# Kernel tuning notes

Hardware: AMD Instinct MI355X
Metric: run time of the kernel (lower is better)

Reference implementation:

```python
import jax, jax.numpy as jnp
import numpy as np

B, T, C, H, N = 4, 4096, 2048, 32, 64
DMIX, DDEC = 32, 64
N_LAYER, LAYER_ID = 24, 12
GN_EPS = 1e-5 * 8.0 ** 2  # eps = 1e-5 * head_size_divisor**2


def setup_inputs() -> dict:
    key = jax.random.key(0)
    ks = jax.random.split(key, 24)
    r01 = LAYER_ID / (N_LAYER - 1)
    r1a0 = 1.0 - LAYER_ID / N_LAYER
    ddd = (np.arange(C, dtype=np.float32) / C).reshape(1, 1, C)
    maa = lambda p: jnp.asarray(1.0 - ddd ** p, dtype=jnp.float32)
    # decay speed schedule (canonical RWKV6, over channel dim)
    n = np.arange(C, dtype=np.float32)
    decay = (-6.0 + 5.0 * (n / (C - 1)) ** (0.7 + 1.3 * r01)).reshape(1, 1, C)
    # time_faaaa zigzag schedule
    m = np.arange(C, dtype=np.float32)
    zig = ((m + 1) % 3 - 1) * 0.1
    faaaa = (r01 * (1 - m / (C - 1)) + zig).reshape(H, N)
    s = 1.0 / np.sqrt(C)
    return {
        "x": jax.random.normal(ks[0], (B, T, C), jnp.float32),
        "shift_state": jax.random.normal(ks[1], (B, C), jnp.float32),
        "wkv_state": jnp.zeros((B, H, N, N), jnp.float32),
        "time_maa_x": maa(r1a0),
        "time_maa_w": maa(r1a0),
        "time_maa_k": maa(r1a0),
        "time_maa_v": jnp.asarray(1.0 - (ddd ** r1a0 + 0.3 * r01), jnp.float32),
        "time_maa_r": maa(0.5 * r1a0),
        "time_maa_g": maa(0.5 * r1a0),
        "time_maa_w1": jax.random.normal(ks[2], (C, 5 * DMIX), jnp.float32) * 0.01,
        "time_maa_w2": jax.random.uniform(ks[3], (5, DMIX, C), jnp.float32, -0.01, 0.01),
        "time_decay": jnp.asarray(decay, jnp.float32),
        "time_decay_w1": jax.random.normal(ks[4], (C, DDEC), jnp.float32) * 0.01,
        "time_decay_w2": jax.random.uniform(ks[5], (DDEC, C), jnp.float32, -0.01, 0.01),
        "time_faaaa": jnp.asarray(faaaa, jnp.float32),
        "Wr": jax.random.normal(ks[6], (C, C), jnp.float32) * s,
        "Wk": jax.random.normal(ks[7], (C, C), jnp.float32) * s,
        "Wv": jax.random.normal(ks[8], (C, C), jnp.float32) * s,
        "Wg": jax.random.normal(ks[9], (C, C), jnp.float32) * s,
        "Wo": jax.random.normal(ks[10], (C, C), jnp.float32) * s,
        "gn_weight": jnp.ones((C,), jnp.float32),
        "gn_bias": jnp.zeros((C,), jnp.float32),
    }


def reference(x, shift_state, wkv_state, time_maa_x, time_maa_w, time_maa_k,
              time_maa_v, time_maa_r, time_maa_g, time_maa_w1, time_maa_w2,
              time_decay, time_decay_w1, time_decay_w2, time_faaaa,
              Wr, Wk, Wv, Wg, Wo, gn_weight, gn_bias):
    b, t, c = x.shape
    # token shift: previous token (seeded by shift_state) minus current
    xx = jnp.concatenate([shift_state[:, None, :], x[:, :-1]], axis=1) - x
    lx = x[:, -1]
    # LoRA token-shift mixing
    xxx = x + xx * time_maa_x
    t5 = jnp.tanh(xxx @ time_maa_w1).reshape(b, t, 5, DMIX)
    mixes = jnp.einsum('btfd,fdc->fbtc', t5, time_maa_w2)
    mw, mk, mv, mr, mg = mixes
    xw = x + xx * (time_maa_w + mw)
    xk = x + xx * (time_maa_k + mk)
    xv = x + xx * (time_maa_v + mv)
    xr = x + xx * (time_maa_r + mr)
    xg = x + xx * (time_maa_g + mg)
    r = xr @ Wr
    k = xk @ Wk
    v = xv @ Wv
    g = jax.nn.silu(xg @ Wg)
    # data-dependent decay via LoRA; wkv6 uses log-decay -exp(w)
    w = time_decay + jnp.tanh(xw @ time_decay_w1) @ time_decay_w2
    glog = -jnp.exp(w)  # [b,t,c]
    to_heads = lambda z: z.reshape(b, t, H, N).transpose(1, 0, 2, 3)  # [t,b,h,n]
    rh, kh, vh, gh = to_heads(r), to_heads(k), to_heads(v), to_heads(glog)
    u = time_faaaa  # [H,N]

    def step(S, inp):
        r_t, k_t, v_t, g_t = inp  # each [b,h,n]
        kv = jnp.einsum('bhk,bhv->bhkv', k_t, v_t)
        o_t = jnp.einsum('bhk,bhkv->bhv', r_t, S + u[None, :, :, None] * kv)
        S = jnp.exp(g_t)[..., None] * S + kv
        return S, o_t

    state, o = jax.lax.scan(step, wkv_state, (rh, kh, vh, gh))
    o = o.transpose(1, 0, 2, 3).reshape(b, t, c)  # [b,t,c]
    # GroupNorm with H groups over channel dim
    og = o.reshape(b, t, H, N)
    mu = og.mean(-1, keepdims=True)
    var = og.var(-1, keepdims=True)
    on = (og - mu) * jax.lax.rsqrt(var + GN_EPS)
    on = on * gn_weight.reshape(H, N) + gn_bias.reshape(H, N)
    out = (on.reshape(b, t, c) * g) @ Wo
    return out, lx, state
```

## Files before the change

kernel.cpp:

```cpp
#include <hip/hip_runtime.h>
#include <hip/hip_bf16.h>
#include <stdint.h>

#define DEV __device__ __forceinline__

typedef __bf16 bf16x8 __attribute__((ext_vector_type(8)));
typedef float f32x4 __attribute__((ext_vector_type(4)));
typedef unsigned short u16x8 __attribute__((ext_vector_type(8)));

constexpr int kB = 4, kT = 4096, kC = 2048, kH = 32, kN = 64;
constexpr int kM = kB * kT;
constexpr int SEGN = 8, TSEG = kT / SEGN, CHN = TSEG / 64;

DEV float bfu2f(unsigned short u) {
  union { uint32_t i; float f; } x; x.i = ((uint32_t)u) << 16; return x.f;
}
DEV unsigned short f2bfu(float f) {
  union { float f; uint32_t i; } x; x.f = f;
  uint32_t r = x.i + 0x7FFFu + ((x.i >> 16) & 1u);
  return (unsigned short)(r >> 16);
}

DEV void gld16(const void* g, void* l) {
  __builtin_amdgcn_global_load_lds(
      (const __attribute__((address_space(1))) void*)g,
      (__attribute__((address_space(3))) void*)l, 16, 0, 0);
}

DEV int swzb(int row, int byteoff) { return (row << 7) + (byteoff ^ ((row & 7) << 4)); }

__global__ __launch_bounds__(256) void trans_bf16(
    const float* __restrict__ in, unsigned short* __restrict__ out, int R, int Cn) {
  __shared__ __attribute__((aligned(16))) unsigned short tile[64][65];
  const int t = threadIdx.x;
  const int r0 = blockIdx.y * 64, c0 = blockIdx.x * 64;
  const int lr = t >> 6, lc = t & 63;
#pragma unroll
  for (int i = 0; i < 16; i++) {
    int rr = lr + i * 4;
    int gr = r0 + rr, gc = c0 + lc;
    if (gr < R && gc < Cn) tile[rr][lc] = f2bfu(in[(size_t)gr * Cn + gc]);
  }
  __syncthreads();
#pragma unroll
  for (int i = 0; i < 16; i++) {
    int cc = lr + i * 4;
    int gc = c0 + cc, gr = r0 + lc;
    if (gc < Cn && gr < R) out[(size_t)gc * R + gr] = tile[lc][cc];
  }
}

__global__ __launch_bounds__(256) void prep_x2(
    const float* __restrict__ x, const float* __restrict__ shift,
    const float* __restrict__ maax,
    unsigned short* __restrict__ xxx, float* __restrict__ lx) {
  size_t i4 = ((size_t)blockIdx.x * 256 + threadIdx.x) * 4;
  int c = (int)(i4 & (kC - 1));
  size_t bt = i4 >> 11;
  int tt = (int)(bt & (kT - 1));
  int b = (int)(bt >> 12);
  float4 xv = *(const float4*)(x + i4);
  float4 pv = (tt == 0) ? *(const float4*)(shift + (size_t)b * kC + c)
                        : *(const float4*)(x + i4 - kC);
  float4 mx = *(const float4*)(maax + c);
  ushort4 o4;
  o4.x = f2bfu(xv.x + (pv.x - xv.x) * mx.x);
  o4.y = f2bfu(xv.y + (pv.y - xv.y) * mx.y);
  o4.z = f2bfu(xv.z + (pv.z - xv.z) * mx.z);
  o4.w = f2bfu(xv.w + (pv.w - xv.w) * mx.w);
  *(ushort4*)(xxx + i4) = o4;
  if (tt == kT - 1) *(float4*)(lx + (size_t)b * kC + c) = xv;
}

enum { E_F32 = 0, E_BF16 = 1, E_TANH = 2, E_SILU = 3, E_DECAY = 4 };

template <int BM, int BN, int EPI>
__global__ __launch_bounds__(256) void gemm_k(
    const unsigned short* __restrict__ A, const unsigned short* __restrict__ Bt,
    void* __restrict__ Cout, const float* __restrict__ aux, int M, int N, int K) {
  constexpr int WGM = (BM == 128 && BN == 128) ? 2 : (BM == 64 ? 2 : 4);
  constexpr int WGN = 4 / WGM;
  constexpr int WM = BM / WGM, WN = BN / WGN;
  constexpr int WR = WM / 16, WC = WN / 16;
  __shared__ __attribute__((aligned(16))) unsigned short As[BM * 32];
  __shared__ __attribute__((aligned(16))) unsigned short Bs[BN * 32];
  const int t = threadIdx.x, wid = t >> 6, l = t & 63;
  const int m0 = blockIdx.x * BM, n0 = blockIdx.y * BN;
  const int wm0 = (wid / WGN) * WM, wn0 = (wid % WGN) * WN;
  f32x4 acc[WR][WC];
#pragma unroll
  for (int i = 0; i < WR; i++)
#pragma unroll
    for (int j = 0; j < WC; j++) acc[i][j] = f32x4{0.f, 0.f, 0.f, 0.f};

  const int rowS = t >> 2, cbS = (t & 3) * 16;
  const char* Ab = (const char*)A;
  const char* Bb = (const char*)Bt;
  const int aoff = (wm0 + (l & 15)) * 32 + (l >> 4) * 8;
  const int boff = (wn0 + (l & 15)) * 32 + (l >> 4) * 8;

  for (int kt = 0; kt < K; kt += 32) {
#pragma unroll
    for (int ia = 0; ia < BM / 64; ia++)
      gld16(Ab + ((size_t)(m0 + ia * 64 + rowS) * K + kt) * 2 + cbS,
            (char*)As + ia * 4096 + wid * 1024);
    if constexpr (BN >= 64) {
#pragma unroll
      for (int ib = 0; ib < BN / 64; ib++)
        gld16(Bb + ((size_t)(n0 + ib * 64 + rowS) * K + kt) * 2 + cbS,
              (char*)Bs + ib * 4096 + wid * 1024);
    } else {
      if (t < BN * 4)
        gld16(Bb + ((size_t)(n0 + rowS) * K + kt) * 2 + cbS,
              (char*)Bs + wid * 1024);
    }
    __syncthreads();
    bf16x8 af[WR], bfv[WC];
#pragma unroll
    for (int mi = 0; mi < WR; mi++) af[mi] = *(const bf16x8*)(&As[aoff + mi * 512]);
#pragma unroll
    for (int ni = 0; ni < WC; ni++) bfv[ni] = *(const bf16x8*)(&Bs[boff + ni * 512]);
#pragma unroll
    for (int mi = 0; mi < WR; mi++)
#pragma unroll
      for (int ni = 0; ni < WC; ni++)
        acc[mi][ni] = __builtin_amdgcn_mfma_f32_16x16x32_bf16(af[mi], bfv[ni], acc[mi][ni], 0, 0, 0);
    __syncthreads();
  }

#pragma unroll
  for (int mi = 0; mi < WR; mi++) {
#pragma unroll
    for (int ni = 0; ni < WC; ni++) {
      int row = m0 + wm0 + mi * 16 + (l >> 4) * 4;
      int col = n0 + wn0 + ni * 16 + (l & 15);
#pragma unroll
      for (int j = 0; j < 4; j++) {
        float v = acc[mi][ni][j];
        size_t idx = (size_t)(row + j) * N + col;
        if constexpr (EPI == E_F32) ((float*)Cout)[idx] = v;
        else if constexpr (EPI == E_BF16) ((unsigned short*)Cout)[idx] = f2bfu(v);
        else if constexpr (EPI == E_TANH) ((unsigned short*)Cout)[idx] = f2bfu(tanhf(v));
        else if constexpr (EPI == E_SILU) ((unsigned short*)Cout)[idx] = f2bfu(v / (1.f + expf(-v)));
        else if constexpr (EPI == E_DECAY) {
          float w = v + aux[col];
          ((float*)Cout)[idx] = expf(-expf(w));
        }
      }
    }
  }
}

DEV void stage256(const unsigned short* A, const unsigned short* Bt,
                  char* lds, int aoff, int boff, int m0, int n0, int K, int kt,
                  int tid, int wid) {
#pragma unroll
  for (int i = 0; i < 4; i++) {
    int row = i * 64 + (tid >> 3);
    int cb = ((tid & 7) * 16) ^ ((row & 7) << 4);
    gld16((const char*)A + ((size_t)(m0 + row) * K + kt) * 2 + cb,
          lds + aoff + i * 8192 + wid * 1024);
    gld16((const char*)Bt + ((size_t)(n0 + row) * K + kt) * 2 + cb,
          lds + boff + i * 8192 + wid * 1024);
  }
}

template <int EPI>
__global__ __launch_bounds__(512, 2) void gemm256_k(
    const unsigned short* __restrict__ A, const unsigned short* __restrict__ Bt,
    void* __restrict__ Cout, int M, int N, int K) {
  extern __shared__ __attribute__((aligned(16))) char lds[];
  const int tid = threadIdx.x, wid = tid >> 6, l = tid & 63;

  const int nwg = gridDim.x, cpx = nwg >> 3;
  int swz = (blockIdx.x & 7) * cpx + (blockIdx.x >> 3);
  const int mtiles = M >> 8;
  const int m0 = (swz % mtiles) * 256, n0 = (swz / mtiles) * 256;

  const int wm = (wid >> 2) * 128, wn = (wid & 3) * 64;
  f32x4 acc[8][4];
#pragma unroll
  for (int i = 0; i < 8; i++)
#pragma unroll
    for (int j = 0; j < 4; j++) acc[i][j] = f32x4{0.f, 0.f, 0.f, 0.f};

  const int KT = K >> 6;
  stage256(A, Bt, lds, 0, 65536, m0, n0, K, 0, tid, wid);
  __syncthreads();
  int cur = 0;

  for (int t = 0; t < KT; ++t) {
    if (t + 1 < KT)
      stage256(A, Bt, lds, (cur ^ 1) * 32768, 65536 + (cur ^ 1) * 32768,
               m0, n0, K, (t + 1) * 64, tid, wid);
    const char* Ab = lds + cur * 32768;
    const char* Bb = lds + 65536 + cur * 32768;
    __builtin_amdgcn_s_setprio(1);
#pragma unroll
    for (int ks = 0; ks < 2; ks++) {
      bf16x8 a[8];
#pragma unroll
      for (int mi = 0; mi < 8; mi++)
        a[mi] = *(const bf16x8*)(Ab + swzb(wm + mi * 16 + (l & 15), ks * 64 + (l >> 4) * 16));
#pragma unroll
      for (int ni = 0; ni < 4; ni++) {
        bf16x8 b = *(const bf16x8*)(Bb + swzb(wn + ni * 16 + (l & 15), ks * 64 + (l >> 4) * 16));
#pragma unroll
        for (int mi = 0; mi < 8; mi++)
          acc[mi][ni] = __builtin_amdgcn_mfma_f32_16x16x32_bf16(a[mi], b, acc[mi][ni], 0, 0, 0);
      }
    }
    __builtin_amdgcn_s_setprio(0);
    __syncthreads();
    cur ^= 1;
  }

#pragma unroll
  for (int mi = 0; mi < 8; mi++)
#pragma unroll
    for (int ni = 0; ni < 4; ni++) {
      int row = m0 + wm + mi * 16 + (l >> 4) * 4;
      int col = n0 + wn + ni * 16 + (l & 15);
#pragma unroll
      for (int j = 0; j < 4; j++) {
        float v = acc[mi][ni][j];
        size_t idx = (size_t)(row + j) * N + col;
        if constexpr (EPI == E_F32) ((float*)Cout)[idx] = v;
        else if constexpr (EPI == E_BF16) ((unsigned short*)Cout)[idx] = f2bfu(v);
        else if constexpr (EPI == E_SILU) ((unsigned short*)Cout)[idx] = f2bfu(v / (1.f + expf(-v)));
      }
    }
}

__global__ __launch_bounds__(256) void mixf_k(
    const unsigned short* __restrict__ t5, const unsigned short* __restrict__ w2t,
    const float* __restrict__ x, const float* __restrict__ shift,
    const float* __restrict__ maa, unsigned short* __restrict__ xout, int f) {
  __shared__ __attribute__((aligned(16))) unsigned short As[64 * 32];
  __shared__ __attribute__((aligned(16))) unsigned short Bs[64 * 32];
  const int t = threadIdx.x, wid = t >> 6, l = t & 63;
  const int m0 = blockIdx.x * 64, n0 = blockIdx.y * 64;
  const int wm0 = (wid >> 1) * 32, wn0 = (wid & 1) * 32;
  const int rowS = t >> 2, cbS = (t & 3) * 16;
  const int aoff = (wm0 + (l & 15)) * 32 + (l >> 4) * 8;
  const int boff = (wn0 + (l & 15)) * 32 + (l >> 4) * 8;

  gld16((const char*)t5 + ((size_t)(m0 + rowS) * 160 + f * 32) * 2 + cbS, (char*)As + wid * 1024);
  gld16((const char*)w2t + ((size_t)(n0 + rowS) * 160 + f * 32) * 2 + cbS, (char*)Bs + wid * 1024);
  __syncthreads();
  bf16x8 a0 = *(const bf16x8*)(&As[aoff]), a1 = *(const bf16x8*)(&As[aoff + 512]);
  bf16x8 b0 = *(const bf16x8*)(&Bs[boff]), b1 = *(const bf16x8*)(&Bs[boff + 512]);
  f32x4 acc[2][2];
  acc[0][0] = f32x4{0.f, 0.f, 0.f, 0.f}; acc[0][1] = f32x4{0.f, 0.f, 0.f, 0.f};
  acc[1][0] = f32x4{0.f, 0.f, 0.f, 0.f}; acc[1][1] = f32x4{0.f, 0.f, 0.f, 0.f};
  acc[0][0] = __builtin_amdgcn_mfma_f32_16x16x32_bf16(a0, b0, acc[0][0], 0, 0, 0);
  acc[0][1] = __builtin_amdgcn_mfma_f32_16x16x32_bf16(a0, b1, acc[0][1], 0, 0, 0);
  acc[1][0] = __builtin_amdgcn_mfma_f32_16x16x32_bf16(a1, b0, acc[1][0], 0, 0, 0);
  acc[1][1] = __builtin_amdgcn_mfma_f32_16x16x32_bf16(a1, b1, acc[1][1], 0, 0, 0);

#pragma unroll
  for (int mi = 0; mi < 2; mi++)
#pragma unroll
    for (int ni = 0; ni < 2; ni++) {
      int row = m0 + wm0 + mi * 16 + (l >> 4) * 4;
      int col = n0 + wn0 + ni * 16 + (l & 15);
      float mv = maa[col];
#pragma unroll
      for (int j = 0; j < 4; j++) {
        int rrow = row + j;
        int tt = rrow & (kT - 1);
        size_t idx = (size_t)rrow * kC + col;
        float xv = x[idx];
        float pv = (tt == 0) ? shift[(size_t)(rrow >> 12) * kC + col] : x[idx - kC];
        xout[idx] = f2bfu(xv + (pv - xv) * (mv + acc[mi][ni][j]));
      }
    }
}

__global__ __launch_bounds__(256) void wkv_local_k(
    const unsigned short* __restrict__ kb, const unsigned short* __restrict__ vb,
    const float* __restrict__ ed, float* __restrict__ Lbuf, float* __restrict__ Dseg) {
  const int bid = blockIdx.x;
  const int bh = bid >> 3, seg = bid & 7;
  const int h = bh & 31, b = bh >> 5;
  const int tid = threadIdx.x, w = tid >> 6, l = tid & 63;
  __shared__ __attribute__((aligned(16))) unsigned short KQks[4096];
  __shared__ __attribute__((aligned(16))) unsigned short Vt[4096];
  __shared__ __attribute__((aligned(16))) float Sf[64][68];
  __shared__ float segp[4][64];
  __shared__ float DLs[64];

  const int fr = l & 15, fq = l >> 4;
#pragma unroll
  for (int ni = 0; ni < 4; ni++)
#pragma unroll
    for (int j = 0; j < 4; j++) Sf[w * 16 + fq * 4 + j][ni * 16 + fr] = 0.f;

  float dtot = 1.f;
  float kv[16], dv[16], vv[16];
  {
    size_t g = ((size_t)b * kT + seg * TSEG + w * 16) * kC + h * 64 + l;
#pragma unroll
    for (int i = 0; i < 16; i++) {
      kv[i] = bfu2f(kb[g]); vv[i] = bfu2f(vb[g]); dv[i] = ed[g];
      g += kC;
    }
  }

  for (int ch = 0; ch < CHN; ++ch) {
    float p = 1.f;
#pragma unroll
    for (int i = 0; i < 16; i++) p *= dv[i];
    segp[w][l] = p;
    __syncthreads();
    float pre = 1.f;
    if (w > 0) pre *= segp[0][l];
    if (w > 1) pre *= segp[1][l];
    if (w > 2) pre *= segp[2][l];
    if (w == 3) DLs[l] = pre * p;

    unsigned short kqrow[16], vtrow[16];
    float run = pre;
#pragma unroll
    for (int i = 0; i < 16; i++) {
      run *= dv[i];
      kqrow[i] = f2bfu(kv[i] / run);
      vtrow[i] = f2bfu(vv[i]);
    }
    {
      u16x8 q0, q1, v0, v1;
#pragma unroll
      for (int j = 0; j < 8; j++) { q0[j] = kqrow[j]; q1[j] = kqrow[j + 8]; v0[j] = vtrow[j]; v1[j] = vtrow[j + 8]; }
      *(u16x8*)((char*)KQks + swzb(l, w * 32)) = q0;
      *(u16x8*)((char*)KQks + swzb(l, w * 32 + 16)) = q1;
      *(u16x8*)((char*)Vt + swzb(l, w * 32)) = v0;
      *(u16x8*)((char*)Vt + swzb(l, w * 32 + 16)) = v1;
    }
    if (ch < CHN - 1) {
      size_t g = ((size_t)b * kT + seg * TSEG + (ch + 1) * 64 + w * 16) * kC + h * 64 + l;
#pragma unroll
      for (int i = 0; i < 16; i++) {
        kv[i] = bfu2f(kb[g]); vv[i] = bfu2f(vb[g]); dv[i] = ed[g];
        g += kC;
      }
    }
    __syncthreads();

    bf16x8 kA0 = *(const bf16x8*)((const char*)KQks + swzb(w * 16 + fr, fq * 16));
    bf16x8 kA1 = *(const bf16x8*)((const char*)KQks + swzb(w * 16 + fr, fq * 16 + 64));
    f32x4 kvacc[4];
#pragma unroll
    for (int ni = 0; ni < 4; ni++) {
      bf16x8 bv0 = *(const bf16x8*)((const char*)Vt + swzb(ni * 16 + fr, fq * 16));
      bf16x8 bv1 = *(const bf16x8*)((const char*)Vt + swzb(ni * 16 + fr, fq * 16 + 64));
      kvacc[ni] = __builtin_amdgcn_mfma_f32_16x16x32_bf16(kA0, bv0, f32x4{0.f, 0.f, 0.f, 0.f}, 0, 0, 0);
      kvacc[ni] = __builtin_amdgcn_mfma_f32_16x16x32_bf16(kA1, bv1, kvacc[ni], 0, 0, 0);
    }
    float dlj[4];
#pragma unroll
    for (int j = 0; j < 4; j++) dlj[j] = DLs[w * 16 + fq * 4 + j];
#pragma unroll
    for (int ni = 0; ni < 4; ni++)
#pragma unroll
      for (int j = 0; j < 4; j++) {
        int kk2 = w * 16 + fq * 4 + j, vv2 = ni * 16 + fr;
        Sf[kk2][vv2] = (Sf[kk2][vv2] + kvacc[ni][j]) * dlj[j];
      }
    dtot *= DLs[l];
    __syncthreads();
  }

  float* Lp = Lbuf + (size_t)bid * 4096;
#pragma unroll
  for (int ni = 0; ni < 4; ni++)
#pragma unroll
    for (int j = 0; j < 4; j++)
      Lp[(size_t)(w * 16 + fq * 4 + j) * 64 + ni * 16 + fr] = Sf[w * 16 + fq * 4 + j][ni * 16 + fr];
  if (w == 0) Dseg[(size_t)bid * 64 + l] = dtot;
}

__global__ __launch_bounds__(256) void wkv_combine_k(
    const float* __restrict__ s0, const float* __restrict__ Dseg,
    float* __restrict__ Lbuf, float* __restrict__ sOut) {
  const int bh = blockIdx.x, tid = threadIdx.x;
  const int k = tid >> 2, v0 = (tid & 3) * 16;
  float4 s[4];
  const float* sp = s0 + (size_t)bh * 4096 + (size_t)k * 64 + v0;
#pragma unroll
  for (int q = 0; q < 4; q++) s[q] = ((const float4*)sp)[q];
  for (int seg = 0; seg < SEGN; ++seg) {
    size_t idx = (size_t)bh * SEGN + seg;
    float d = Dseg[idx * 64 + k];
    float* Lp = Lbuf + idx * 4096 + (size_t)k * 64 + v0;
#pragma unroll
    for (int q = 0; q < 4; q++) {
      float4 lq = ((float4*)Lp)[q];
      ((float4*)Lp)[q] = s[q];
      s[q].x = d * s[q].x + lq.x; s[q].y = d * s[q].y + lq.y;
      s[q].z = d * s[q].z + lq.z; s[q].w = d * s[q].w + lq.w;
    }
  }
  float* op = sOut + (size_t)bh * 4096 + (size_t)k * 64 + v0;
#pragma unroll
  for (int q = 0; q < 4; q++) ((float4*)op)[q] = s[q];
}

__global__ __launch_bounds__(256) void wkv_seg_k(
    const unsigned short* __restrict__ rb, const unsigned short* __restrict__ kb,
    const unsigned short* __restrict__ vb, const float* __restrict__ ed,
    const float* __restrict__ uf, const float* __restrict__ Sini,
    unsigned short* __restrict__ o) {
  const int bid = blockIdx.x;
  const int bh = bid >> 3, seg = bid & 7;
  const int h = bh & 31, b = bh >> 5;
  const int tid = threadIdx.x, w = tid >> 6, l = tid & 63;
  __shared__ __attribute__((aligned(16))) unsigned short RQ[4096];
  __shared__ __attribute__((aligned(16))) unsigned short KQsk[4096];
  __shared__ __attribute__((aligned(16))) unsigned short KQks[4096];
  __shared__ __attribute__((aligned(16))) unsigned short Vt[4096];
  __shared__ __attribute__((aligned(16))) unsigned short Pl[4096];
  __shared__ __attribute__((aligned(16))) unsigned short S0T[4096];
  __shared__ __attribute__((aligned(16))) float Sf[64][68];
  __shared__ float segp[4][64];
  __shared__ float DLs[64];
  __shared__ float diag[64];

  const float uu = uf[h * 64 + l];

  {
    int k0 = tid >> 2, vs = (tid & 3) << 4;
    const float* sp = Sini + (size_t)bid * 4096 + (size_t)k0 * 64 + vs;
#pragma unroll
    for (int q = 0; q < 4; q++) {
      float4 f4 = ((const float4*)sp)[q];
      int v = vs + q * 4;
      Sf[k0][v + 0] = f4.x; Sf[k0][v + 1] = f4.y; Sf[k0][v + 2] = f4.z; Sf[k0][v + 3] = f4.w;
      *(unsigned short*)((char*)S0T + swzb(v + 0, k0 * 2)) = f2bfu(f4.x);
      *(unsigned short*)((char*)S0T + swzb(v + 1, k0 * 2)) = f2bfu(f4.y);
      *(unsigned short*)((char*)S0T + swzb(v + 2, k0 * 2)) = f2bfu(f4.z);
      *(unsigned short*)((char*)S0T + swzb(v + 3, k0 * 2)) = f2bfu(f4.w);
    }
  }
  __syncthreads();

  const int fr = l & 15, fq = l >> 4;
  float rv[16], kv[16], dv[16], vv[16];

  {
    size_t g = ((size_t)b * kT + seg * TSEG + w * 16) * kC + h * 64 + l;
#pragma unroll
    for (int i = 0; i < 16; i++) {
      rv[i] = bfu2f(rb[g]); kv[i] = bfu2f(kb[g]); vv[i] = bfu2f(vb[g]); dv[i] = ed[g];
      g += kC;
    }
  }

  for (int ch = 0; ch < CHN; ++ch) {
    float p = 1.f;
#pragma unroll
    for (int i = 0; i < 16; i++) p *= dv[i];
    segp[w][l] = p;
    __syncthreads();
    float pre = 1.f;
    if (w > 0) pre *= segp[0][l];
    if (w > 1) pre *= segp[1][l];
    if (w > 2) pre *= segp[2][l];
    if (w == 3) DLs[l] = pre * p;

    unsigned short kqrow[16], vtrow[16];
    float run = pre;
#pragma unroll
    for (int i = 0; i < 16; i++) {
      int t = w * 16 + i;
      float rq = rv[i] * run;
      run *= dv[i];
      float kq = kv[i] / run;
      *(unsigned short*)((char*)RQ + swzb(t, l * 2)) = f2bfu(rq);
      unsigned short kqu = f2bfu(kq);
      *(unsigned short*)((char*)KQsk + swzb(t, l * 2)) = kqu;
      kqrow[i] = kqu;
      vtrow[i] = f2bfu(vv[i]);
    }
    {
      u16x8 q0, q1, v0, v1;
#pragma unroll
      for (int j = 0; j < 8; j++) { q0[j] = kqrow[j]; q1[j] = kqrow[j + 8]; v0[j] = vtrow[j]; v1[j] = vtrow[j + 8]; }
      *(u16x8*)((char*)KQks + swzb(l, w * 32)) = q0;
      *(u16x8*)((char*)KQks + swzb(l, w * 32 + 16)) = q1;
      *(u16x8*)((char*)Vt + swzb(l, w * 32)) = v0;
      *(u16x8*)((char*)Vt + swzb(l, w * 32 + 16)) = v1;
    }
#pragma unroll
    for (int i = 0; i < 16; i++) {
      float dsv = rv[i] * uu * kv[i];
#pragma unroll
      for (int m = 1; m < 64; m <<= 1) dsv += __shfl_xor(dsv, m, 64);
      if (l == 0) diag[w * 16 + i] = dsv;
    }

    if (ch < CHN - 1) {
      size_t g = ((size_t)b * kT + seg * TSEG + (ch + 1) * 64 + w * 16) * kC + h * 64 + l;
#pragma unroll
      for (int i = 0; i < 16; i++) {
        rv[i] = bfu2f(rb[g]); kv[i] = bfu2f(kb[g]); vv[i] = bfu2f(vb[g]); dv[i] = ed[g];
        g += kC;
      }
    }
    __syncthreads();

    bf16x8 a0 = *(const bf16x8*)((const char*)RQ + swzb(w * 16 + fr, fq * 16));
    bf16x8 a1 = *(const bf16x8*)((const char*)RQ + swzb(w * 16 + fr, fq * 16 + 64));
    f32x4 pacc[4];
#pragma unroll
    for (int ni = 0; ni < 4; ni++) {
      bf16x8 b0 = *(const bf16x8*)((const char*)KQsk + swzb(ni * 16 + fr, fq * 16));
      bf16x8 b1 = *(const bf16x8*)((const char*)KQsk + swzb(ni * 16 + fr, fq * 16 + 64));
      pacc[ni] = __builtin_amdgcn_mfma_f32_16x16x32_bf16(a0, b0, f32x4{0.f, 0.f, 0.f, 0.f}, 0, 0, 0);
      pacc[ni] = __builtin_amdgcn_mfma_f32_16x16x32_bf16(a1, b1, pacc[ni], 0, 0, 0);
    }
    float dg[4];
#pragma unroll
    for (int j = 0; j < 4; j++) dg[j] = diag[w * 16 + fq * 4 + j];
#pragma unroll
    for (int ni = 0; ni < 4; ni++)
#pragma unroll
      for (int j = 0; j < 4; j++) {
        int row = w * 16 + fq * 4 + j, col = ni * 16 + fr;
        float pv = pacc[ni][j];
        pv = (col < row) ? pv : ((col == row) ? dg[j] : 0.f);
        *(unsigned short*)((char*)Pl + swzb(row, col * 2)) = f2bfu(pv);
      }
    __syncthreads();

    bf16x8 pA0 = *(const bf16x8*)((const char*)Pl + swzb(w * 16 + fr, fq * 16));
    bf16x8 pA1 = *(const bf16x8*)((const char*)Pl + swzb(w * 16 + fr, fq * 16 + 64));
    bf16x8 kA0 = *(const bf16x8*)((const char*)KQks + swzb(w * 16 + fr, fq * 16));
    bf16x8 kA1 = *(const bf16x8*)((const char*)KQks + swzb(w * 16 + fr, fq * 16 + 64));
    f32x4 oacc[4], kvacc[4];
#pragma unroll
    for (int ni = 0; ni < 4; ni++) {
      bf16x8 bv0 = *(const bf16x8*)((const char*)Vt + swzb(ni * 16 + fr, fq * 16));
      bf16x8 bv1 = *(const bf16x8*)((const char*)Vt + swzb(ni * 16 + fr, fq * 16 + 64));
      bf16x8 bs0 = *(const bf16x8*)((const char*)S0T + swzb(ni * 16 + fr, fq * 16));
      bf16x8 bs1 = *(const bf16x8*)((const char*)S0T + swzb(ni * 16 + fr, fq * 16 + 64));
      oacc[ni] = __builtin_amdgcn_mfma_f32_16x16x32_bf16(pA0, bv0, f32x4{0.f, 0.f, 0.f, 0.f}, 0, 0, 0);
      oacc[ni] = __builtin_amdgcn_mfma_f32_16x16x32_bf16(pA1, bv1, oacc[ni], 0, 0, 0);
      oacc[ni] = __builtin_amdgcn_mfma_f32_16x16x32_bf16(a0, bs0, oacc[ni], 0, 0, 0);
      oacc[ni] = __builtin_amdgcn_mfma_f32_16x16x32_bf16(a1, bs1, oacc[ni], 0, 0, 0);
      kvacc[ni] = __builtin_amdgcn_mfma_f32_16x16x32_bf16(kA0, bv0, f32x4{0.f, 0.f, 0.f, 0.f}, 0, 0, 0);
      kvacc[ni] = __builtin_amdgcn_mfma_f32_16x16x32_bf16(kA1, bv1, kvacc[ni], 0, 0, 0);
    }
    size_t obase = ((size_t)b * kT + seg * TSEG + ch * 64) * kC + h * 64;
#pragma unroll
    for (int ni = 0; ni < 4; ni++)
#pragma unroll
      for (int j = 0; j < 4; j++)
        o[obase + (size_t)(w * 16 + fq * 4 + j) * kC + ni * 16 + fr] = f2bfu(oacc[ni][j]);
    __syncthreads();

    float dlj[4];
#pragma unroll
    for (int j = 0; j < 4; j++) dlj[j] = DLs[w * 16 + fq * 4 + j];
#pragma unroll
    for (int ni = 0; ni < 4; ni++)
#pragma unroll
      for (int j = 0; j < 4; j++) {
        int kk2 = w * 16 + fq * 4 + j, vv2 = ni * 16 + fr;
        float sn = (Sf[kk2][vv2] + kvacc[ni][j]) * dlj[j];
        Sf[kk2][vv2] = sn;
        *(unsigned short*)((char*)S0T + swzb(vv2, kk2 * 2)) = f2bfu(sn);
      }
    __syncthreads();
  }
}

__global__ __launch_bounds__(256) void gn_k(
    const unsigned short* __restrict__ o, const unsigned short* __restrict__ gb,
    const float* __restrict__ gnw, const float* __restrict__ gnb,
    unsigned short* __restrict__ y) {
  int gi = blockIdx.x * 4 + (threadIdx.x >> 6);
  int j = threadIdx.x & 63;
  int bt = gi >> 5, h = gi & 31;
  size_t idx = (size_t)bt * kC + h * 64 + j;
  float val = bfu2f(o[idx]);
  float s = val, s2 = val * val;
#pragma unroll
  for (int m = 1; m < 64; m <<= 1) {
    s += __shfl_xor(s, m, 64);
    s2 += __shfl_xor(s2, m, 64);
  }
  float mu = s * 0.015625f;
  float var = s2 * 0.015625f - mu * mu;
  float rs = rsqrtf(var + 6.4e-4f);
  float on = (val - mu) * rs * gnw[h * 64 + j] + gnb[h * 64 + j];
  y[idx] = f2bfu(on * bfu2f(gb[idx]));
}

constexpr size_t SZW     = (size_t)2048 * 2048 * 2;
constexpr size_t OFF_WRT = 0;
constexpr size_t OFF_WKT = 1 * SZW;
constexpr size_t OFF_WVT = 2 * SZW;
constexpr size_t OFF_WGT = 3 * SZW;
constexpr size_t OFF_WOT = 4 * SZW;
constexpr size_t OFF_W1T = 5 * SZW;
constexpr size_t OFF_W2T = OFF_W1T + (size_t)160 * 2048 * 2;
constexpr size_t OFF_TD1 = OFF_W2T + (size_t)2048 * 160 * 2;
constexpr size_t OFF_TD2 = OFF_TD1 + (size_t)64 * 2048 * 2;
constexpr size_t OFF_T5  = OFF_TD2 + (size_t)2048 * 64 * 2;
constexpr size_t OFF_DT  = OFF_T5 + (size_t)kM * 160 * 2;
constexpr size_t OFF_EDEC= OFF_DT + (size_t)kM * 64 * 2;
constexpr size_t OFF_XMIX= OFF_EDEC + (size_t)kM * kC * 4;
constexpr size_t OFF_R   = OFF_XMIX + (size_t)kM * kC * 2;
constexpr size_t OFF_K   = OFF_R + (size_t)kM * kC * 2;
constexpr size_t OFF_V   = OFF_K + (size_t)kM * kC * 2;
constexpr size_t OFF_L   = OFF_WRT;

extern "C" void kernel_launch(void* const* d_in, const int* in_sizes, int n_in,
                              void* d_out, int out_size, void* d_ws, size_t ws_size,
                              hipStream_t stream) {
  const float* x     = (const float*)d_in[0];
  const float* shift = (const float*)d_in[1];
  const float* s0    = (const float*)d_in[2];
  const float* maax  = (const float*)d_in[3];
  const float* maaw  = (const float*)d_in[4];
  const float* maak  = (const float*)d_in[5];
  const float* maav  = (const float*)d_in[6];
  const float* maar  = (const float*)d_in[7];
  const float* maag  = (const float*)d_in[8];
  const float* w1    = (const float*)d_in[9];
  const float* w2    = (const float*)d_in[10];
  const float* tdec  = (const float*)d_in[11];
  const float* tdw1  = (const float*)d_in[12];
  const float* tdw2  = (const float*)d_in[13];
  const float* faaaa = (const float*)d_in[14];
  const float* Wr    = (const float*)d_in[15];
  const float* Wk    = (const float*)d_in[16];
  const float* Wv    = (const float*)d_in[17];
  const float* Wg    = (const float*)d_in[18];
  const float* Wo    = (const float*)d_in[19];
  const float* gnw   = (const float*)d_in[20];
  const float* gnb   = (const float*)d_in[21];

  char* ws = (char*)d_ws;
  unsigned short* Wrt  = (unsigned short*)(ws + OFF_WRT);
  unsigned short* Wkt  = (unsigned short*)(ws + OFF_WKT);
  unsigned short* Wvt  = (unsigned short*)(ws + OFF_WVT);
  unsigned short* Wgt  = (unsigned short*)(ws + OFF_WGT);
  unsigned short* Wot  = (unsigned short*)(ws + OFF_WOT);
  unsigned short* w1t  = (unsigned short*)(ws + OFF_W1T);
  unsigned short* w2t  = (unsigned short*)(ws + OFF_W2T);
  unsigned short* td1t = (unsigned short*)(ws + OFF_TD1);
  unsigned short* td2t = (unsigned short*)(ws + OFF_TD2);
  unsigned short* t5   = (unsigned short*)(ws + OFF_T5);
  unsigned short* dtmp = (unsigned short*)(ws + OFF_DT);
  float*          edec = (float*)(ws + OFF_EDEC);
  unsigned short* xg   = (unsigned short*)(ws + OFF_EDEC);
  unsigned short* xmix = (unsigned short*)(ws + OFF_XMIX);
  unsigned short* obf  = (unsigned short*)(ws + OFF_XMIX);
  unsigned short* rbb  = (unsigned short*)(ws + OFF_R);
  unsigned short* gbb  = (unsigned short*)(ws + OFF_R);
  unsigned short* kbb  = (unsigned short*)(ws + OFF_K);
  unsigned short* ybuf = (unsigned short*)(ws + OFF_K);
  unsigned short* vbb  = (unsigned short*)(ws + OFF_V);
  float*          Lbuf = (float*)(ws + OFF_L);
  float*          DsegP= (float*)(ws + OFF_TD1);

  float* outp  = (float*)d_out;
  float* lx    = outp + (size_t)kM * kC;
  float* stOut = lx + (size_t)kB * kC;

  dim3 blk(256);

  trans_bf16<<<dim3(32, 32), blk, 0, stream>>>(Wr, Wrt, 2048, 2048);
  trans_bf16<<<dim3(32, 32), blk, 0, stream>>>(Wk, Wkt, 2048, 2048);
  trans_bf16<<<dim3(32, 32), blk, 0, stream>>>(Wv, Wvt, 2048, 2048);
  trans_bf16<<<dim3(32, 32), blk, 0, stream>>>(Wg, Wgt, 2048, 2048);
  trans_bf16<<<dim3(32, 32), blk, 0, stream>>>(Wo, Wot, 2048, 2048);
  trans_bf16<<<dim3(3, 32), blk, 0, stream>>>(w1, w1t, 2048, 160);
  trans_bf16<<<dim3(1, 32), blk, 0, stream>>>(tdw1, td1t, 2048, 64);
  trans_bf16<<<dim3(32, 1), blk, 0, stream>>>(tdw2, td2t, 64, 2048);
  trans_bf16<<<dim3(32, 3), blk, 0, stream>>>(w2, w2t, 160, 2048);

  prep_x2<<<dim3(kM * kC / 4 / 256), blk, 0, stream>>>(x, shift, maax, xmix, lx);

  gemm_k<128, 32, E_TANH><<<dim3(kM / 128, 5), blk, 0, stream>>>(xmix, w1t, t5, nullptr, kM, 160, 2048);

  dim3 mgrid(kM / 64, kC / 64);
  constexpr int G256 = (kM / 256) * (kC / 256);
  constexpr size_t LDS256 = 131072;

  mixf_k<<<mgrid, blk, 0, stream>>>(t5, w2t, x, shift, maaw, xmix, 0);
  gemm_k<64, 64, E_TANH><<<dim3(kM / 64, 1), blk, 0, stream>>>(xmix, td1t, dtmp, nullptr, kM, 64, 2048);
  gemm_k<128, 128, E_DECAY><<<dim3(kM / 128, 16), blk, 0, stream>>>(dtmp, td2t, edec, tdec, kM, 2048, 64);

  mixf_k<<<mgrid, blk, 0, stream>>>(t5, w2t, x, shift, maak, xmix, 1);
  gemm256_k<E_BF16><<<dim3(G256), dim3(512), LDS256, stream>>>(xmix, Wkt, kbb, kM, 2048, 2048);
  mixf_k<<<mgrid, blk, 0, stream>>>(t5, w2t, x, shift, maav, xmix, 2);
  gemm256_k<E_BF16><<<dim3(G256), dim3(512), LDS256, stream>>>(xmix, Wvt, vbb, kM, 2048, 2048);
  mixf_k<<<mgrid, blk, 0, stream>>>(t5, w2t, x, shift, maar, xmix, 3);
  gemm256_k<E_BF16><<<dim3(G256), dim3(512), LDS256, stream>>>(xmix, Wrt, rbb, kM, 2048, 2048);

  wkv_local_k<<<dim3(kB * kH * SEGN), blk, 0, stream>>>(kbb, vbb, edec, Lbuf, DsegP);
  wkv_combine_k<<<dim3(kB * kH), blk, 0, stream>>>(s0, DsegP, Lbuf, stOut);
  wkv_seg_k<<<dim3(kB * kH * SEGN), blk, 0, stream>>>(rbb, kbb, vbb, edec, faaaa, Lbuf, obf);

  mixf_k<<<mgrid, blk, 0, stream>>>(t5, w2t, x, shift, maag, xg, 4);
  gemm256_k<E_SILU><<<dim3(G256), dim3(512), LDS256, stream>>>(xg, Wgt, gbb, kM, 2048, 2048);

  gn_k<<<dim3(kM * kH / 4), blk, 0, stream>>>(obf, gbb, gnw, gnb, ybuf);

  gemm256_k<E_F32><<<dim3(G256), dim3(512), LDS256, stream>>>(ybuf, Wot, outp, kM, 2048, 2048);
}
```

Baseline: 1.533 ms.

## Pipeline GEMM loads with partial waitcnt, keep WKV state in registers, MFMA diagonal

```diff
diff --git a/kernel.cpp b/kernel.cpp
--- a/kernel.cpp
+++ b/kernel.cpp
@@ -186,16 +186,46 @@
 
   const int KT = K >> 6;
   stage256(A, Bt, lds, 0, 65536, m0, n0, K, 0, tid, wid);
-  __syncthreads();
   int cur = 0;
 
-  for (int t = 0; t < KT; ++t) {
-    if (t + 1 < KT)
-      stage256(A, Bt, lds, (cur ^ 1) * 32768, 65536 + (cur ^ 1) * 32768,
-               m0, n0, K, (t + 1) * 64, tid, wid);
+  for (int t = 0; t < KT - 1; ++t) {
+    stage256(A, Bt, lds, (cur ^ 1) * 32768, 65536 + (cur ^ 1) * 32768,
+             m0, n0, K, (t + 1) * 64, tid, wid);
+    asm volatile("s_waitcnt vmcnt(8)" ::: "memory");
+    __builtin_amdgcn_s_barrier();
+    __builtin_amdgcn_sched_barrier(0);
+    {
+      const char* Ab = lds + cur * 32768;
+      const char* Bb = lds + 65536 + cur * 32768;
+      __builtin_amdgcn_s_setprio(1);
+#pragma unroll
+      for (int ks = 0; ks < 2; ks++) {
+        bf16x8 a[8];
+#pragma unroll
+        for (int mi = 0; mi < 8; mi++)
+          a[mi] = *(const bf16x8*)(Ab + swzb(wm + mi * 16 + (l & 15), ks * 64 + (l >> 4) * 16));
+#pragma unroll
+        for (int ni = 0; ni < 4; ni++) {
+          bf16x8 b = *(const bf16x8*)(Bb + swzb(wn + ni * 16 + (l & 15), ks * 64 + (l >> 4) * 16));
+#pragma unroll
+          for (int mi = 0; mi < 8; mi++)
+            acc[mi][ni] = __builtin_amdgcn_mfma_f32_16x16x32_bf16(a[mi], b, acc[mi][ni], 0, 0, 0);
+        }
+      }
+      __builtin_amdgcn_s_setprio(0);
+    }
+    asm volatile("s_waitcnt lgkmcnt(0)" ::: "memory");
+    __builtin_amdgcn_s_barrier();
+    __builtin_amdgcn_sched_barrier(0);
+    cur ^= 1;
+  }
+
+  asm volatile("s_waitcnt vmcnt(0)" ::: "memory");
+  __builtin_amdgcn_s_barrier();
+  __builtin_amdgcn_sched_barrier(0);
+  {
     const char* Ab = lds + cur * 32768;
     const char* Bb = lds + 65536 + cur * 32768;
-    __builtin_amdgcn_s_setprio(1);
 #pragma unroll
     for (int ks = 0; ks < 2; ks++) {
       bf16x8 a[8];
@@ -210,9 +240,6 @@
           acc[mi][ni] = __builtin_amdgcn_mfma_f32_16x16x32_bf16(a[mi], b, acc[mi][ni], 0, 0, 0);
       }
     }
-    __builtin_amdgcn_s_setprio(0);
-    __syncthreads();
-    cur ^= 1;
   }
 
 #pragma unroll
@@ -286,15 +313,13 @@
   const int tid = threadIdx.x, w = tid >> 6, l = tid & 63;
   __shared__ __attribute__((aligned(16))) unsigned short KQks[4096];
   __shared__ __attribute__((aligned(16))) unsigned short Vt[4096];
-  __shared__ __attribute__((aligned(16))) float Sf[64][68];
   __shared__ float segp[4][64];
   __shared__ float DLs[64];
 
   const int fr = l & 15, fq = l >> 4;
-#pragma unroll
-  for (int ni = 0; ni < 4; ni++)
-#pragma unroll
-    for (int j = 0; j < 4; j++) Sf[w * 16 + fq * 4 + j][ni * 16 + fr] = 0.f;
+  f32x4 Sreg[4];
+#pragma unroll
+  for (int ni = 0; ni < 4; ni++) Sreg[ni] = f32x4{0.f, 0.f, 0.f, 0.f};
 
   float dtot = 1.f;
   float kv[16], dv[16], vv[16];
@@ -362,10 +387,8 @@
 #pragma unroll
     for (int ni = 0; ni < 4; ni++)
 #pragma unroll
-      for (int j = 0; j < 4; j++) {
-        int kk2 = w * 16 + fq * 4 + j, vv2 = ni * 16 + fr;
-        Sf[kk2][vv2] = (Sf[kk2][vv2] + kvacc[ni][j]) * dlj[j];
-      }
+      for (int j = 0; j < 4; j++)
+        Sreg[ni][j] = (Sreg[ni][j] + kvacc[ni][j]) * dlj[j];
     dtot *= DLs[l];
     __syncthreads();
   }
@@ -375,7 +398,7 @@
   for (int ni = 0; ni < 4; ni++)
 #pragma unroll
     for (int j = 0; j < 4; j++)
-      Lp[(size_t)(w * 16 + fq * 4 + j) * 64 + ni * 16 + fr] = Sf[w * 16 + fq * 4 + j][ni * 16 + fr];
+      Lp[(size_t)(w * 16 + fq * 4 + j) * 64 + ni * 16 + fr] = Sreg[ni][j];
   if (w == 0) Dseg[(size_t)bid * 64 + l] = dtot;
 }
 
@@ -420,32 +443,27 @@
   __shared__ __attribute__((aligned(16))) unsigned short Vt[4096];
   __shared__ __attribute__((aligned(16))) unsigned short Pl[4096];
   __shared__ __attribute__((aligned(16))) unsigned short S0T[4096];
-  __shared__ __attribute__((aligned(16))) float Sf[64][68];
+  __shared__ __attribute__((aligned(16))) unsigned short RU[4096];
+  __shared__ __attribute__((aligned(16))) unsigned short Ksk[4096];
   __shared__ float segp[4][64];
   __shared__ float DLs[64];
-  __shared__ float diag[64];
 
   const float uu = uf[h * 64 + l];
-
-  {
-    int k0 = tid >> 2, vs = (tid & 3) << 4;
-    const float* sp = Sini + (size_t)bid * 4096 + (size_t)k0 * 64 + vs;
-#pragma unroll
-    for (int q = 0; q < 4; q++) {
-      float4 f4 = ((const float4*)sp)[q];
-      int v = vs + q * 4;
-      Sf[k0][v + 0] = f4.x; Sf[k0][v + 1] = f4.y; Sf[k0][v + 2] = f4.z; Sf[k0][v + 3] = f4.w;
-      *(unsigned short*)((char*)S0T + swzb(v + 0, k0 * 2)) = f2bfu(f4.x);
-      *(unsigned short*)((char*)S0T + swzb(v + 1, k0 * 2)) = f2bfu(f4.y);
-      *(unsigned short*)((char*)S0T + swzb(v + 2, k0 * 2)) = f2bfu(f4.z);
-      *(unsigned short*)((char*)S0T + swzb(v + 3, k0 * 2)) = f2bfu(f4.w);
-    }
-  }
+  const int fr = l & 15, fq = l >> 4;
+
+  f32x4 Sreg[4];
+#pragma unroll
+  for (int ni = 0; ni < 4; ni++)
+#pragma unroll
+    for (int j = 0; j < 4; j++) {
+      int kk2 = w * 16 + fq * 4 + j, vv2 = ni * 16 + fr;
+      float sv = Sini[(size_t)bid * 4096 + (size_t)kk2 * 64 + vv2];
+      Sreg[ni][j] = sv;
+      *(unsigned short*)((char*)S0T + swzb(vv2, kk2 * 2)) = f2bfu(sv);
+    }
   __syncthreads();
 
-  const int fr = l & 15, fq = l >> 4;
   float rv[16], kv[16], dv[16], vv[16];
-
   {
     size_t g = ((size_t)b * kT + seg * TSEG + w * 16) * kC + h * 64 + l;
 #pragma unroll
@@ -476,6 +494,8 @@
       run *= dv[i];
       float kq = kv[i] / run;
       *(unsigned short*)((char*)RQ + swzb(t, l * 2)) = f2bfu(rq);
+      *(unsigned short*)((char*)RU + swzb(t, l * 2)) = f2bfu(rv[i] * uu);
+      *(unsigned short*)((char*)Ksk + swzb(t, l * 2)) = f2bfu(kv[i]);
       unsigned short kqu = f2bfu(kq);
       *(unsigned short*)((char*)KQsk + swzb(t, l * 2)) = kqu;
       kqrow[i] = kqu;
@@ -490,13 +510,6 @@
       *(u16x8*)((char*)Vt + swzb(l, w * 32)) = v0;
       *(u16x8*)((char*)Vt + swzb(l, w * 32 + 16)) = v1;
     }
-#pragma unroll
-    for (int i = 0; i < 16; i++) {
-      float dsv = rv[i] * uu * kv[i];
-#pragma unroll
-      for (int m = 1; m < 64; m <<= 1) dsv += __shfl_xor(dsv, m, 64);
-      if (l == 0) diag[w * 16 + i] = dsv;
-    }
 
     if (ch < CHN - 1) {
       size_t g = ((size_t)b * kT + seg * TSEG + (ch + 1) * 64 + w * 16) * kC + h * 64 + l;
@@ -518,9 +531,18 @@
       pacc[ni] = __builtin_amdgcn_mfma_f32_16x16x32_bf16(a0, b0, f32x4{0.f, 0.f, 0.f, 0.f}, 0, 0, 0);
       pacc[ni] = __builtin_amdgcn_mfma_f32_16x16x32_bf16(a1, b1, pacc[ni], 0, 0, 0);
     }
+    f32x4 dacc;
+    {
+      bf16x8 ru0 = *(const bf16x8*)((const char*)RU + swzb(w * 16 + fr, fq * 16));
+      bf16x8 ru1 = *(const bf16x8*)((const char*)RU + swzb(w * 16 + fr, fq * 16 + 64));
+      bf16x8 kb0 = *(const bf16x8*)((const char*)Ksk + swzb(w * 16 + fr, fq * 16));
+      bf16x8 kb1 = *(const bf16x8*)((const char*)Ksk + swzb(w * 16 + fr, fq * 16 + 64));
+      dacc = __builtin_amdgcn_mfma_f32_16x16x32_bf16(ru0, kb0, f32x4{0.f, 0.f, 0.f, 0.f}, 0, 0, 0);
+      dacc = __builtin_amdgcn_mfma_f32_16x16x32_bf16(ru1, kb1, dacc, 0, 0, 0);
+    }
     float dg[4];
 #pragma unroll
-    for (int j = 0; j < 4; j++) dg[j] = diag[w * 16 + fq * 4 + j];
+    for (int j = 0; j < 4; j++) dg[j] = __shfl(dacc[j], fq * 20 + j, 64);
 #pragma unroll
     for (int ni = 0; ni < 4; ni++)
 #pragma unroll
@@ -566,8 +588,8 @@
 #pragma unroll
       for (int j = 0; j < 4; j++) {
         int kk2 = w * 16 + fq * 4 + j, vv2 = ni * 16 + fr;
-        float sn = (Sf[kk2][vv2] + kvacc[ni][j]) * dlj[j];
-        Sf[kk2][vv2] = sn;
+        float sn = (Sreg[ni][j] + kvacc[ni][j]) * dlj[j];
+        Sreg[ni][j] = sn;
         *(unsigned short*)((char*)S0T + swzb(vv2, kk2 * 2)) = f2bfu(sn);
       }
     __syncthreads();
```

Result: slower. 1.577 ms (+2.9%).
